# Performance work log

Hardware: AMD Instinct MI355X
Metric: run time of the kernel (lower is better)

## Reference

```python
import math
import jax, jax.numpy as jnp
import numpy as np

N = 100000
E_RAND = 800000
IN_F, HID, OUT_F, HEADS = 128, 64, 64, 4
NOISE_SCALE = 1.0 * math.sqrt(2.0 * math.log(1.25 / 0.05))  # dp_rate=1, eps=1, del=0.05


def setup_inputs() -> dict:
    key = jax.random.key(0)
    ks = jax.random.split(key, 12)
    x = jax.random.normal(ks[0], (N, IN_F), dtype=jnp.float32)
    src_r = jax.random.randint(ks[1], (E_RAND,), 0, N, dtype=jnp.int32)
    dst_r = jax.random.randint(ks[2], (E_RAND,), 0, N, dtype=jnp.int32)
    loops = jnp.arange(N, dtype=jnp.int32)  # add_self_loop
    src = jnp.concatenate([src_r, loops])
    dst = jnp.concatenate([dst_r, loops])
    # layer 0: GATConv(in=128, out=64, heads=4)
    s0 = 1.0 / math.sqrt(IN_F)
    W0 = jax.random.normal(ks[3], (IN_F, HEADS * HID), dtype=jnp.float32) * s0
    al0 = jax.random.normal(ks[4], (HEADS, HID), dtype=jnp.float32) * 0.1
    ar0 = jax.random.normal(ks[5], (HEADS, HID), dtype=jnp.float32) * 0.1
    b0 = jnp.zeros((HEADS * HID,), dtype=jnp.float32)
    # layer 1: GATConv(in=256, out=64, heads=1)
    s1 = 1.0 / math.sqrt(HEADS * HID)
    W1 = jax.random.normal(ks[6], (HEADS * HID, OUT_F), dtype=jnp.float32) * s1
    al1 = jax.random.normal(ks[7], (1, OUT_F), dtype=jnp.float32) * 0.1
    ar1 = jax.random.normal(ks[8], (1, OUT_F), dtype=jnp.float32) * 0.1
    b1 = jnp.zeros((OUT_F,), dtype=jnp.float32)
    # DP gaussian noise added after first GAT layer (torch.normal(0,1,x.shape))
    noise = jax.random.normal(ks[9], (N, HEADS * HID), dtype=jnp.float32)
    return {"x": x, "src": src, "dst": dst, "W0": W0, "al0": al0, "ar0": ar0,
            "b0": b0, "W1": W1, "al1": al1, "ar1": ar1, "b1": b1, "noise": noise}


def gat_conv(x, src, dst, W, al, ar, b, apply_act):
    """DGL GATConv: per-edge attention, edge softmax over dst, scatter-sum."""
    H, D = al.shape
    h = (x @ W).reshape(-1, H, D)                      # [N,H,D]
    el = jnp.sum(h * al, axis=-1)                      # [N,H]
    er = jnp.sum(h * ar, axis=-1)                      # [N,H]
    e = jax.nn.leaky_relu(el[src] + er[dst], 0.2)      # [E,H]
    emax = jax.ops.segment_max(e, dst, num_segments=N) # [N,H]
    a = jnp.exp(e - emax[dst])
    denom = jax.ops.segment_sum(a, dst, num_segments=N)
    alpha = a / denom[dst]                             # [E,H] edge softmax
    msg = h[src] * alpha[:, :, None]                   # [E,H,D]
    out = jax.ops.segment_sum(msg, dst, num_segments=N) + b.reshape(1, H, D)
    if apply_act:
        out = jax.nn.leaky_relu(out, 0.01)             # F.leaky_relu default slope
    return out.reshape(-1, H * D)                      # flatten(1)


def reference(x, src, dst, W0, al0, ar0, b0, W1, al1, ar1, b1, noise):
    h = gat_conv(x, src, dst, W0, al0, ar0, b0, apply_act=True)   # [N, 256]
    h = h + NOISE_SCALE * noise                                   # DP noise after layer 0
    out = gat_conv(h, src, dst, W1, al1, ar1, b1, apply_act=False)  # [N, 64]
    return out
```

## Files before the change

### kernel.cpp

```cpp
#include <hip/hip_runtime.h>
#include <hip/hip_bf16.h>
#include <math.h>

#define IN_F 128
#define HID 64
#define HEADS 4
#define HD0 (HEADS * HID)
#define OUT_F 64
#define NOISE_SCALE 2.5372725354060904f

typedef __bf16 bf16x8 __attribute__((ext_vector_type(8)));
typedef float f32x4 __attribute__((ext_vector_type(4)));
typedef float f4 __attribute__((ext_vector_type(4)));
typedef unsigned int u4 __attribute__((ext_vector_type(4)));

__device__ __forceinline__ float bf2f(unsigned short u) {
    return __uint_as_float(((unsigned)u) << 16);
}
__device__ __forceinline__ unsigned short f2bf(float f) {
    unsigned u = __float_as_uint(f);
    u = u + 0x7fffu + ((u >> 16) & 1u);
    return (unsigned short)(u >> 16);
}

__device__ __forceinline__ void acc8(float* acc, const uint4& u, float wt) {
    acc[0] += wt * __uint_as_float(u.x << 16);
    acc[1] += wt * __uint_as_float(u.x & 0xffff0000u);
    acc[2] += wt * __uint_as_float(u.y << 16);
    acc[3] += wt * __uint_as_float(u.y & 0xffff0000u);
    acc[4] += wt * __uint_as_float(u.z << 16);
    acc[5] += wt * __uint_as_float(u.z & 0xffff0000u);
    acc[6] += wt * __uint_as_float(u.w << 16);
    acc[7] += wt * __uint_as_float(u.w & 0xffff0000u);
}

__global__ __launch_bounds__(256) void prep_kernel(
    const float* __restrict__ in, unsigned short* __restrict__ out, size_t n8,
    int* __restrict__ deg, int N, int nb_cast,
    const float* __restrict__ W0, unsigned short* __restrict__ W0t,
    const float* __restrict__ W1, unsigned short* __restrict__ W1t) {
    const int b = blockIdx.x;
    if (b < nb_cast) {
        size_t i = (size_t)b * 256 + threadIdx.x;
        if (i < (size_t)N) deg[i] = 0;
        if (i >= n8) return;
        const f4 a = __builtin_nontemporal_load((const f4*)in + i * 2);
        const f4 c = __builtin_nontemporal_load((const f4*)in + i * 2 + 1);
        ushort4 o0, o1;
        o0.x = f2bf(a.x); o0.y = f2bf(a.y); o0.z = f2bf(a.z); o0.w = f2bf(a.w);
        o1.x = f2bf(c.x); o1.y = f2bf(c.y); o1.z = f2bf(c.z); o1.w = f2bf(c.w);
        ((ushort4*)out)[i * 2] = o0;
        ((ushort4*)out)[i * 2 + 1] = o1;
    } else if (b < nb_cast + (IN_F * HD0) / 256) {
        int i = (b - nb_cast) * 256 + threadIdx.x;
        int n = i / IN_F, k = i % IN_F;
        W0t[i] = f2bf(W0[(size_t)k * HD0 + n]);
    } else {
        int j = (b - nb_cast - (IN_F * HD0) / 256) * 256 + threadIdx.x;
        if (j < HD0 * OUT_F) {
            int n = j / HD0, k = j % HD0;
            W1t[j] = f2bf(W1[(size_t)k * OUT_F + n]);
        }
    }
}

template <int K, int H, int NT>
__global__ __launch_bounds__(256) void gemm_fused_kernel(
    const unsigned short* __restrict__ A, const unsigned short* __restrict__ Bt,
    unsigned short* __restrict__ C, const float* __restrict__ al,
    const float* __restrict__ ar, float* __restrict__ el,
    float* __restrict__ er, int M, int NC) {
    constexpr int KH = (K > 128) ? 128 : K;
    constexpr int BSTR = K + 8;
    constexpr int ASTR = KH + 8;
    constexpr int NROWS = 64 * NT;
    __shared__ __align__(16) unsigned short Bs[NROWS * BSTR];
    __shared__ __align__(16) unsigned short As[128 * ASTR];
    const int tid = threadIdx.x;
    const int lane = tid & 63, w = tid >> 6;
    const int row0 = blockIdx.y * 128;
    const int n0 = blockIdx.x * NROWS;
    for (int i = tid; i < NROWS * (K / 8); i += 256) {
        int n = i / (K / 8), kc = i % (K / 8);
        *(uint4*)(Bs + n * BSTR + kc * 8) =
            *(const uint4*)(Bt + (size_t)(n0 + n) * K + kc * 8);
    }
    f32x4 acc[2][4 * NT] = {};
    const int q = lane >> 4, c = lane & 15;
    for (int kh = 0; kh < K; kh += KH) {
        __syncthreads();
        for (int i = tid; i < 128 * (KH / 8); i += 256) {
            int r = i / (KH / 8), kc = i % (KH / 8);
            uint4 v = make_uint4(0, 0, 0, 0);
            int gr = row0 + r;
            if (gr < M) v = *(const uint4*)(A + (size_t)gr * K + kh + kc * 8);
            *(uint4*)(As + r * ASTR + kc * 8) = v;
        }
        __syncthreads();
#pragma unroll
        for (int k0 = 0; k0 < KH; k0 += 32) {
            bf16x8 af[2], bfr[4 * NT];
            af[0] = *(const bf16x8*)(As + (w * 32 + c) * ASTR + k0 + q * 8);
            af[1] = *(const bf16x8*)(As + (w * 32 + 16 + c) * ASTR + k0 + q * 8);
#pragma unroll
            for (int nt = 0; nt < 4 * NT; ++nt)
                bfr[nt] = *(const bf16x8*)(Bs + (nt * 16 + c) * BSTR + kh + k0 + q * 8);
#pragma unroll
            for (int mt = 0; mt < 2; ++mt)
#pragma unroll
                for (int nt = 0; nt < 4 * NT; ++nt)
                    acc[mt][nt] = __builtin_amdgcn_mfma_f32_16x16x32_bf16(
                        af[mt], bfr[nt], acc[mt][nt], 0, 0, 0);
        }
    }
    float alv[4 * NT], arv[4 * NT];
#pragma unroll
    for (int nt = 0; nt < 4 * NT; ++nt) {
        alv[nt] = al[n0 + nt * 16 + c];
        arv[nt] = ar[n0 + nt * 16 + c];
    }
    const int headbase = n0 >> 6;
#pragma unroll
    for (int mt = 0; mt < 2; ++mt) {
#pragma unroll
        for (int r = 0; r < 4; ++r) {
            int grow = row0 + w * 32 + mt * 16 + q * 4 + r;
            bool ok = grow < M;
#pragma unroll
            for (int g = 0; g < NT; ++g) {
                float elp = 0.f, erp = 0.f;
#pragma unroll
                for (int t = 0; t < 4; ++t) {
                    int nt = g * 4 + t;
                    float v = acc[mt][nt][r];
                    elp += v * alv[nt];
                    erp += v * arv[nt];
                    if (ok) C[(size_t)grow * NC + n0 + nt * 16 + c] = f2bf(v);
                }
#pragma unroll
                for (int o = 8; o > 0; o >>= 1) {
                    elp += __shfl_down(elp, o, 16);
                    erp += __shfl_down(erp, o, 16);
                }
                if (c == 0 && ok) {
                    el[(size_t)grow * H + headbase + g] = elp;
                    er[(size_t)grow * H + headbase + g] = erp;
                }
            }
        }
    }
}

__global__ __launch_bounds__(256) void degree_kernel(
    const int* __restrict__ dst, int* __restrict__ deg, int E) {
    int e = blockIdx.x * 256 + threadIdx.x;
    if (e < E) atomicAdd(&deg[dst[e]], 1);
}

__global__ __launch_bounds__(256) void scan_block_kernel(
    const int* __restrict__ deg, int* __restrict__ off,
    int* __restrict__ bsum, int N) {
    __shared__ int s[256];
    int i = blockIdx.x * 256 + threadIdx.x;
    int v = (i < N) ? deg[i] : 0;
    s[threadIdx.x] = v;
    __syncthreads();
    for (int d = 1; d < 256; d <<= 1) {
        int t = (threadIdx.x >= d) ? s[threadIdx.x - d] : 0;
        __syncthreads();
        s[threadIdx.x] += t;
        __syncthreads();
    }
    if (i < N) off[i] = s[threadIdx.x] - v;
    if (threadIdx.x == 255) bsum[blockIdx.x] = s[255];
}

__global__ __launch_bounds__(256) void add_offsets_kernel(
    int* __restrict__ off, int* __restrict__ cur,
    const int* __restrict__ bsum, int N, int E) {
    __shared__ int sred[4];
    int partial = 0;
    for (int i = threadIdx.x; i < blockIdx.x; i += 256) partial += bsum[i];
#pragma unroll
    for (int o = 32; o > 0; o >>= 1) partial += __shfl_down(partial, o);
    if ((threadIdx.x & 63) == 0) sred[threadIdx.x >> 6] = partial;
    __syncthreads();
    int base = sred[0] + sred[1] + sred[2] + sred[3];
    int i = blockIdx.x * 256 + threadIdx.x;
    if (i < N) {
        int v = off[i] + base;
        off[i] = v;
        cur[i] = v;
    }
    if (i == 0) off[N] = E;
}

__global__ __launch_bounds__(256) void fill_csr_kernel(
    const int* __restrict__ src, const int* __restrict__ dst,
    int* __restrict__ cur, int* __restrict__ csr_src, int E) {
    int e = blockIdx.x * 256 + threadIdx.x;
    if (e >= E) return;
    int d = dst[e];
    int pos = atomicAdd(&cur[d], 1);
    csr_src[pos] = src[e];
}

__global__ __launch_bounds__(256) void agg0_kernel(
    const int* __restrict__ off, const int* __restrict__ csr_src,
    const unsigned short* __restrict__ h,
    const float* __restrict__ el,
    const float* __restrict__ er,
    const float* __restrict__ b0, const float* __restrict__ noise,
    unsigned short* __restrict__ out, int N) {
    int gt = blockIdx.x * 256 + threadIdx.x;
    int n = gt >> 5;
    if (n >= N) return;
    const int lane = gt & 31;
    const int hd = lane >> 3;
    const int f0 = lane << 3;
    const float ern = er[(size_t)n * 4 + hd];
    const int beg = off[n];
    const int last = off[n + 1] - 1;
    float acc[8] = {0.f, 0.f, 0.f, 0.f, 0.f, 0.f, 0.f, 0.f};
    float l = 0.f;
    for (int p = beg; p <= last; p += 4) {
        int i1 = p + 1, i2 = p + 2, i3 = p + 3;
        const bool v1 = i1 <= last, v2 = i2 <= last, v3 = i3 <= last;
        i1 = v1 ? i1 : last;
        i2 = v2 ? i2 : last;
        i3 = v3 ? i3 : last;
        const int s0 = csr_src[p],  s1 = csr_src[i1];
        const int s2 = csr_src[i2], s3 = csr_src[i3];
        float e0 = el[(size_t)s0 * 4 + hd] + ern;
        float e1 = el[(size_t)s1 * 4 + hd] + ern;
        float e2 = el[(size_t)s2 * 4 + hd] + ern;
        float e3 = el[(size_t)s3 * 4 + hd] + ern;
        const uint4 u0 = *(const uint4*)(h + (size_t)s0 * HD0 + f0);
        const uint4 u1 = *(const uint4*)(h + (size_t)s1 * HD0 + f0);
        const uint4 u2 = *(const uint4*)(h + (size_t)s2 * HD0 + f0);
        const uint4 u3 = *(const uint4*)(h + (size_t)s3 * HD0 + f0);
        e0 = e0 > 0.f ? e0 : 0.2f * e0;
        e1 = e1 > 0.f ? e1 : 0.2f * e1;
        e2 = e2 > 0.f ? e2 : 0.2f * e2;
        e3 = e3 > 0.f ? e3 : 0.2f * e3;
        const float w0 = __expf(e0);
        const float w1 = v1 ? __expf(e1) : 0.f;
        const float w2 = v2 ? __expf(e2) : 0.f;
        const float w3 = v3 ? __expf(e3) : 0.f;
        acc8(acc, u0, w0);
        acc8(acc, u1, w1);
        acc8(acc, u2, w2);
        acc8(acc, u3, w3);
        l += (w0 + w1) + (w2 + w3);
    }
    const float rd = 1.f / l;
    const float4 ba = *(const float4*)(b0 + f0);
    const float4 bb = *(const float4*)(b0 + f0 + 4);
    const f4 na = __builtin_nontemporal_load((const f4*)(noise + (size_t)n * HD0 + f0));
    const f4 nb = __builtin_nontemporal_load((const f4*)(noise + (size_t)n * HD0 + f0 + 4));
    float o[8];
    o[0] = acc[0] * rd + ba.x;
    o[1] = acc[1] * rd + ba.y;
    o[2] = acc[2] * rd + ba.z;
    o[3] = acc[3] * rd + ba.w;
    o[4] = acc[4] * rd + bb.x;
    o[5] = acc[5] * rd + bb.y;
    o[6] = acc[6] * rd + bb.z;
    o[7] = acc[7] * rd + bb.w;
#pragma unroll
    for (int j = 0; j < 8; ++j) o[j] = o[j] > 0.f ? o[j] : 0.01f * o[j];
    o[0] += NOISE_SCALE * na.x;
    o[1] += NOISE_SCALE * na.y;
    o[2] += NOISE_SCALE * na.z;
    o[3] += NOISE_SCALE * na.w;
    o[4] += NOISE_SCALE * nb.x;
    o[5] += NOISE_SCALE * nb.y;
    o[6] += NOISE_SCALE * nb.z;
    o[7] += NOISE_SCALE * nb.w;
    u4 ov;
    ov.x = (unsigned)f2bf(o[0]) | ((unsigned)f2bf(o[1]) << 16);
    ov.y = (unsigned)f2bf(o[2]) | ((unsigned)f2bf(o[3]) << 16);
    ov.z = (unsigned)f2bf(o[4]) | ((unsigned)f2bf(o[5]) << 16);
    ov.w = (unsigned)f2bf(o[6]) | ((unsigned)f2bf(o[7]) << 16);
    __builtin_nontemporal_store(ov, (u4*)(out + (size_t)n * HD0 + f0));
}

__global__ __launch_bounds__(256) void agg1_kernel(
    const int* __restrict__ off, const int* __restrict__ csr_src,
    const unsigned short* __restrict__ h,
    const float* __restrict__ el,
    const float* __restrict__ er,
    const float* __restrict__ b1, float* __restrict__ out, int N) {
    int gt = blockIdx.x * 256 + threadIdx.x;
    int n = gt >> 4;
    if (n >= N) return;
    const int lane = gt & 15;
    const int f0 = lane << 2;
    const float ern = er[n];
    const int beg = off[n];
    const int last = off[n + 1] - 1;
    float a0 = 0.f, a1 = 0.f, a2 = 0.f, a3 = 0.f, l = 0.f;
    for (int p = beg; p <= last; p += 4) {
        int i1 = p + 1, i2 = p + 2, i3 = p + 3;
        const bool v1 = i1 <= last, v2 = i2 <= last, v3 = i3 <= last;
        i1 = v1 ? i1 : last;
        i2 = v2 ? i2 : last;
        i3 = v3 ? i3 : last;
        const int s0 = csr_src[p],  s1 = csr_src[i1];
        const int s2 = csr_src[i2], s3 = csr_src[i3];
        float e0 = el[s0] + ern;
        float e1 = el[s1] + ern;
        float e2 = el[s2] + ern;
        float e3 = el[s3] + ern;
        const ushort4 u0 = *(const ushort4*)(h + (size_t)s0 * 64 + f0);
        const ushort4 u1 = *(const ushort4*)(h + (size_t)s1 * 64 + f0);
        const ushort4 u2 = *(const ushort4*)(h + (size_t)s2 * 64 + f0);
        const ushort4 u3 = *(const ushort4*)(h + (size_t)s3 * 64 + f0);
        e0 = e0 > 0.f ? e0 : 0.2f * e0;
        e1 = e1 > 0.f ? e1 : 0.2f * e1;
        e2 = e2 > 0.f ? e2 : 0.2f * e2;
        e3 = e3 > 0.f ? e3 : 0.2f * e3;
        const float w0 = __expf(e0);
        const float w1 = v1 ? __expf(e1) : 0.f;
        const float w2 = v2 ? __expf(e2) : 0.f;
        const float w3 = v3 ? __expf(e3) : 0.f;
        a0 += w0 * bf2f(u0.x) + w1 * bf2f(u1.x) + w2 * bf2f(u2.x) + w3 * bf2f(u3.x);
        a1 += w0 * bf2f(u0.y) + w1 * bf2f(u1.y) + w2 * bf2f(u2.y) + w3 * bf2f(u3.y);
        a2 += w0 * bf2f(u0.z) + w1 * bf2f(u1.z) + w2 * bf2f(u2.z) + w3 * bf2f(u3.z);
        a3 += w0 * bf2f(u0.w) + w1 * bf2f(u1.w) + w2 * bf2f(u2.w) + w3 * bf2f(u3.w);
        l += (w0 + w1) + (w2 + w3);
    }
    const float rd = 1.f / l;
    const float4 bv = *(const float4*)(b1 + f0);
    f4 o;
    o.x = a0 * rd + bv.x;
    o.y = a1 * rd + bv.y;
    o.z = a2 * rd + bv.z;
    o.w = a3 * rd + bv.w;
    __builtin_nontemporal_store(o, (f4*)(out + (size_t)n * 64 + f0));
}

extern "C" void kernel_launch(void* const* d_in, const int* in_sizes, int n_in,
                              void* d_out, int out_size, void* d_ws, size_t ws_size,
                              hipStream_t stream) {
    const float* x     = (const float*)d_in[0];
    const int*   src   = (const int*)d_in[1];
    const int*   dst   = (const int*)d_in[2];
    const float* W0    = (const float*)d_in[3];
    const float* al0   = (const float*)d_in[4];
    const float* ar0   = (const float*)d_in[5];
    const float* b0    = (const float*)d_in[6];
    const float* W1    = (const float*)d_in[7];
    const float* al1   = (const float*)d_in[8];
    const float* ar1   = (const float*)d_in[9];
    const float* b1    = (const float*)d_in[10];
    const float* noise = (const float*)d_in[11];

    const int N = in_sizes[0] / IN_F;
    const int E = in_sizes[1];
    const int NB = (N + 255) / 256;

    char* p = (char*)d_ws;
    unsigned short* x_bf   = (unsigned short*)p; p += (size_t)N * IN_F * 2;
    unsigned short* h0     = (unsigned short*)p; p += (size_t)N * HD0 * 2;
    unsigned short* agg0b  = (unsigned short*)p; p += (size_t)N * HD0 * 2;
    unsigned short* h1     = (unsigned short*)p; p += (size_t)N * OUT_F * 2;
    unsigned short* W0t    = (unsigned short*)p; p += (size_t)IN_F * HD0 * 2;
    unsigned short* W1t    = (unsigned short*)p; p += (size_t)HD0 * OUT_F * 2;
    float* el     = (float*)p; p += (size_t)N * HEADS * 4;
    float* er     = (float*)p; p += (size_t)N * HEADS * 4;
    int* deg    = (int*)p; p += (size_t)N * 4;
    int* cur    = (int*)p; p += (size_t)N * 4;
    int* off    = (int*)p; p += ((size_t)N + 4) * 4;
    int* bsum   = (int*)p; p += 512 * 4;
    int* csr_src= (int*)p; p += (size_t)E * 4;

    {
        size_t n8 = (size_t)N * IN_F / 8;
        int nb_cast = (int)((n8 + 255) / 256);
        int nb_w0 = (IN_F * HD0) / 256;
        int nb_w1 = (HD0 * OUT_F + 255) / 256;
        prep_kernel<<<nb_cast + nb_w0 + nb_w1, 256, 0, stream>>>(
            x, x_bf, n8, deg, N, nb_cast, W0, W0t, W1, W1t);
    }

    degree_kernel<<<(E + 255) / 256, 256, 0, stream>>>(dst, deg, E);
    scan_block_kernel<<<NB, 256, 0, stream>>>(deg, off, bsum, N);
    add_offsets_kernel<<<NB, 256, 0, stream>>>(off, cur, bsum, N, E);
    fill_csr_kernel<<<(E + 255) / 256, 256, 0, stream>>>(src, dst, cur, csr_src, E);

    const int MB = (N + 127) / 128;

    {
        dim3 grid(HD0 / 128, MB);
        gemm_fused_kernel<IN_F, HEADS, 2><<<grid, 256, 0, stream>>>(
            x_bf, W0t, h0, al0, ar0, el, er, N, HD0);
    }
    agg0_kernel<<<(unsigned)(((size_t)N * 32 + 255) / 256), 256, 0, stream>>>(
        off, csr_src, h0, el, er, b0, noise, agg0b, N);

    {
        dim3 grid(OUT_F / 64, MB);
        gemm_fused_kernel<HD0, 1, 1><<<grid, 256, 0, stream>>>(
            agg0b, W1t, h1, al1, ar1, el, er, N, OUT_F);
    }
    agg1_kernel<<<(unsigned)(((size_t)N * 16 + 255) / 256), 256, 0, stream>>>(
        off, csr_src, h1, el, er, b1, (float*)d_out, N);
}
```

Before: 456.9 us.

## Move DP noise add into layer-1 GEMM A-load and restage A per k-step

The noise addition moves out of the layer-0 aggregation kernel and into the A-tile load of the layer-1 GEMM. There the bf16 activations are unpacked, noise is added in fp32, and the values are repacked to bf16 before staging in shared memory. The GEMM A staging also changes from large K-halves to a 32-wide k-slice per iteration, with global loads issued before the barrier to overlap them with the previous slice. The intent is to take noise loads off the latency-bound gather kernel and use smaller LDS tiles. The cost is one extra bf16 rounding before noise is added, more barriers in the GEMM, and noise reads moved into the GEMM.

```diff
diff --git a/kernel.cpp b/kernel.cpp
--- a/kernel.cpp
+++ b/kernel.cpp
@@ -32,6 +32,25 @@
     acc[5] += wt * __uint_as_float(u.z & 0xffff0000u);
     acc[6] += wt * __uint_as_float(u.w << 16);
     acc[7] += wt * __uint_as_float(u.w & 0xffff0000u);
+}
+
+__device__ __forceinline__ uint4 addnoise8(uint4 v, const float* np) {
+    const f4 n0 = __builtin_nontemporal_load((const f4*)np);
+    const f4 n1 = __builtin_nontemporal_load((const f4*)(np + 4));
+    float g0 = bf2f((unsigned short)(v.x & 0xffffu)) + NOISE_SCALE * n0.x;
+    float g1 = bf2f((unsigned short)(v.x >> 16))     + NOISE_SCALE * n0.y;
+    float g2 = bf2f((unsigned short)(v.y & 0xffffu)) + NOISE_SCALE * n0.z;
+    float g3 = bf2f((unsigned short)(v.y >> 16))     + NOISE_SCALE * n0.w;
+    float g4 = bf2f((unsigned short)(v.z & 0xffffu)) + NOISE_SCALE * n1.x;
+    float g5 = bf2f((unsigned short)(v.z >> 16))     + NOISE_SCALE * n1.y;
+    float g6 = bf2f((unsigned short)(v.w & 0xffffu)) + NOISE_SCALE * n1.z;
+    float g7 = bf2f((unsigned short)(v.w >> 16))     + NOISE_SCALE * n1.w;
+    uint4 r;
+    r.x = (unsigned)f2bf(g0) | ((unsigned)f2bf(g1) << 16);
+    r.y = (unsigned)f2bf(g2) | ((unsigned)f2bf(g3) << 16);
+    r.z = (unsigned)f2bf(g4) | ((unsigned)f2bf(g5) << 16);
+    r.w = (unsigned)f2bf(g6) | ((unsigned)f2bf(g7) << 16);
+    return r;
 }
 
 __global__ __launch_bounds__(256) void prep_kernel(
@@ -64,15 +83,15 @@
     }
 }
 
-template <int K, int H, int NT>
+template <int K, int H, int NT, bool ADDN>
 __global__ __launch_bounds__(256) void gemm_fused_kernel(
     const unsigned short* __restrict__ A, const unsigned short* __restrict__ Bt,
+    const float* __restrict__ nz,
     unsigned short* __restrict__ C, const float* __restrict__ al,
     const float* __restrict__ ar, float* __restrict__ el,
     float* __restrict__ er, int M, int NC) {
-    constexpr int KH = (K > 128) ? 128 : K;
     constexpr int BSTR = K + 8;
-    constexpr int ASTR = KH + 8;
+    constexpr int ASTR = 40;
     constexpr int NROWS = 64 * NT;
     __shared__ __align__(16) unsigned short Bs[NROWS * BSTR];
     __shared__ __align__(16) unsigned short As[128 * ASTR];
@@ -87,31 +106,36 @@
     }
     f32x4 acc[2][4 * NT] = {};
     const int q = lane >> 4, c = lane & 15;
-    for (int kh = 0; kh < K; kh += KH) {
-        __syncthreads();
-        for (int i = tid; i < 128 * (KH / 8); i += 256) {
-            int r = i / (KH / 8), kc = i % (KH / 8);
-            uint4 v = make_uint4(0, 0, 0, 0);
-            int gr = row0 + r;
-            if (gr < M) v = *(const uint4*)(A + (size_t)gr * K + kh + kc * 8);
-            *(uint4*)(As + r * ASTR + kc * 8) = v;
+    const int r_st = tid >> 1, hh = tid & 1;
+    for (int k0 = 0; k0 < K; k0 += 32) {
+        int gr = row0 + r_st;
+        uint4 av0 = make_uint4(0, 0, 0, 0), av1 = make_uint4(0, 0, 0, 0);
+        if (gr < M) {
+            const unsigned short* ap = A + (size_t)gr * K + k0 + hh * 16;
+            av0 = *(const uint4*)(ap);
+            av1 = *(const uint4*)(ap + 8);
+            if (ADDN) {
+                const float* np_ = nz + (size_t)gr * K + k0 + hh * 16;
+                av0 = addnoise8(av0, np_);
+                av1 = addnoise8(av1, np_ + 8);
+            }
         }
         __syncthreads();
-#pragma unroll
-        for (int k0 = 0; k0 < KH; k0 += 32) {
-            bf16x8 af[2], bfr[4 * NT];
-            af[0] = *(const bf16x8*)(As + (w * 32 + c) * ASTR + k0 + q * 8);
-            af[1] = *(const bf16x8*)(As + (w * 32 + 16 + c) * ASTR + k0 + q * 8);
+        *(uint4*)(As + r_st * ASTR + hh * 16) = av0;
+        *(uint4*)(As + r_st * ASTR + hh * 16 + 8) = av1;
+        __syncthreads();
+        bf16x8 af[2], bfr[4 * NT];
+        af[0] = *(const bf16x8*)(As + (w * 32 + c) * ASTR + q * 8);
+        af[1] = *(const bf16x8*)(As + (w * 32 + 16 + c) * ASTR + q * 8);
+#pragma unroll
+        for (int nt = 0; nt < 4 * NT; ++nt)
+            bfr[nt] = *(const bf16x8*)(Bs + (nt * 16 + c) * BSTR + k0 + q * 8);
+#pragma unroll
+        for (int mt = 0; mt < 2; ++mt)
 #pragma unroll
             for (int nt = 0; nt < 4 * NT; ++nt)
-                bfr[nt] = *(const bf16x8*)(Bs + (nt * 16 + c) * BSTR + kh + k0 + q * 8);
-#pragma unroll
-            for (int mt = 0; mt < 2; ++mt)
-#pragma unroll
-                for (int nt = 0; nt < 4 * NT; ++nt)
-                    acc[mt][nt] = __builtin_amdgcn_mfma_f32_16x16x32_bf16(
-                        af[mt], bfr[nt], acc[mt][nt], 0, 0, 0);
-        }
+                acc[mt][nt] = __builtin_amdgcn_mfma_f32_16x16x32_bf16(
+                    af[mt], bfr[nt], acc[mt][nt], 0, 0, 0);
     }
     float alv[4 * NT], arv[4 * NT];
 #pragma unroll
@@ -210,7 +234,7 @@
     const unsigned short* __restrict__ h,
     const float* __restrict__ el,
     const float* __restrict__ er,
-    const float* __restrict__ b0, const float* __restrict__ noise,
+    const float* __restrict__ b0,
     unsigned short* __restrict__ out, int N) {
     int gt = blockIdx.x * 256 + threadIdx.x;
     int n = gt >> 5;
@@ -256,8 +280,6 @@
     const float rd = 1.f / l;
     const float4 ba = *(const float4*)(b0 + f0);
     const float4 bb = *(const float4*)(b0 + f0 + 4);
-    const f4 na = __builtin_nontemporal_load((const f4*)(noise + (size_t)n * HD0 + f0));
-    const f4 nb = __builtin_nontemporal_load((const f4*)(noise + (size_t)n * HD0 + f0 + 4));
     float o[8];
     o[0] = acc[0] * rd + ba.x;
     o[1] = acc[1] * rd + ba.y;
@@ -269,14 +291,6 @@
     o[7] = acc[7] * rd + bb.w;
 #pragma unroll
     for (int j = 0; j < 8; ++j) o[j] = o[j] > 0.f ? o[j] : 0.01f * o[j];
-    o[0] += NOISE_SCALE * na.x;
-    o[1] += NOISE_SCALE * na.y;
-    o[2] += NOISE_SCALE * na.z;
-    o[3] += NOISE_SCALE * na.w;
-    o[4] += NOISE_SCALE * nb.x;
-    o[5] += NOISE_SCALE * nb.y;
-    o[6] += NOISE_SCALE * nb.z;
-    o[7] += NOISE_SCALE * nb.w;
     u4 ov;
     ov.x = (unsigned)f2bf(o[0]) | ((unsigned)f2bf(o[1]) << 16);
     ov.y = (unsigned)f2bf(o[2]) | ((unsigned)f2bf(o[3]) << 16);
@@ -393,16 +407,16 @@
 
     {
         dim3 grid(HD0 / 128, MB);
-        gemm_fused_kernel<IN_F, HEADS, 2><<<grid, 256, 0, stream>>>(
-            x_bf, W0t, h0, al0, ar0, el, er, N, HD0);
+        gemm_fused_kernel<IN_F, HEADS, 2, false><<<grid, 256, 0, stream>>>(
+            x_bf, W0t, nullptr, h0, al0, ar0, el, er, N, HD0);
     }
     agg0_kernel<<<(unsigned)(((size_t)N * 32 + 255) / 256), 256, 0, stream>>>(
-        off, csr_src, h0, el, er, b0, noise, agg0b, N);
+        off, csr_src, h0, el, er, b0, agg0b, N);
 
     {
         dim3 grid(OUT_F / 64, MB);
-        gemm_fused_kernel<HD0, 1, 1><<<grid, 256, 0, stream>>>(
-            agg0b, W1t, h1, al1, ar1, el, er, N, OUT_F);
+        gemm_fused_kernel<HD0, 1, 1, true><<<grid, 256, 0, stream>>>(
+            agg0b, W1t, noise, h1, al1, ar1, el, er, N, OUT_F);
     }
     agg1_kernel<<<(unsigned)(((size_t)N * 16 + 255) / 256), 256, 0, stream>>>(
         off, csr_src, h1, el, er, b1, (float*)d_out, N);
```

After: 458.3 us. About the same (+0.3%).
